# Optimization experiments

Hardware: AMD Instinct MI355X
Metric: run time of the kernel (lower is better)

The kernel has to match this reference:

```python
import jax, jax.numpy as jnp
import numpy as np

B, S, HID = 2, 4096, 640
NH, NKV, HD = 4, 1, 256
SCALING = 256.0 ** -0.5
SOFTCAP = 50.0
WINDOW = 512
EPS = 1e-6
ROPE_THETA = 10000.0  # local (sliding) rope base in Gemma3


def _rope_tables(seq_len, dim, theta):
    inv_freq = 1.0 / (theta ** (np.arange(0, dim, 2, dtype=np.float32) / dim))  # [dim/2]
    t = np.arange(seq_len, dtype=np.float32)
    freqs = np.outer(t, inv_freq)                      # [S, dim/2]
    emb = np.concatenate([freqs, freqs], axis=-1)      # [S, dim]
    return np.cos(emb)[None], np.sin(emb)[None]        # [1, S, dim]


def _sliding_causal_mask(b, s, window):
    i = np.arange(s)[:, None]
    j = np.arange(s)[None, :]
    allowed = (j <= i) & (j > i - window)              # causal + sliding window
    mask = np.where(allowed, 0.0, -1e9).astype(np.float32)
    return np.broadcast_to(mask[None, None], (b, 1, s, s)).copy()


def setup_inputs() -> dict:
    key = jax.random.key(0)
    ks = jax.random.split(key, 8)
    cos_np, sin_np = _rope_tables(S, HD, ROPE_THETA)
    return {
        "hidden_states": jax.random.normal(ks[0], (B, S, HID), jnp.float32),
        "cos": jnp.asarray(cos_np),
        "sin": jnp.asarray(sin_np),
        "attention_mask": jnp.asarray(_sliding_causal_mask(B, S, WINDOW)),
        "Wq": jax.random.normal(ks[1], (HID, NH * HD), jnp.float32) * 0.02,
        "Wk": jax.random.normal(ks[2], (HID, NKV * HD), jnp.float32) * 0.02,
        "Wv": jax.random.normal(ks[3], (HID, NKV * HD), jnp.float32) * 0.02,
        "Wo": jax.random.normal(ks[4], (NH * HD, HID), jnp.float32) * 0.02,
        "q_norm_w": jax.random.normal(ks[5], (HD,), jnp.float32) * 0.02,
        "k_norm_w": jax.random.normal(ks[6], (HD,), jnp.float32) * 0.02,
    }


def _rms_norm(x, w):
    var = jnp.mean(jnp.square(x), axis=-1, keepdims=True)
    return x * jax.lax.rsqrt(var + EPS) * (1.0 + w)


def _rotate_half(x):
    x1, x2 = jnp.split(x, 2, axis=-1)
    return jnp.concatenate([-x2, x1], axis=-1)


def _apply_rope(x, cos, sin):
    # x: [B, H, S, D]; cos/sin: [1, S, D] -> unsqueeze head dim
    c = cos[:, None, :, :]
    s = sin[:, None, :, :]
    return x * c + _rotate_half(x) * s


def reference(hidden_states, cos, sin, attention_mask, Wq, Wk, Wv, Wo, q_norm_w, k_norm_w):
    b, s, _ = hidden_states.shape
    # projections (no bias)
    q = (hidden_states @ Wq).reshape(b, s, NH, HD).transpose(0, 2, 1, 3)   # [B,NH,S,D]
    k = (hidden_states @ Wk).reshape(b, s, NKV, HD).transpose(0, 2, 1, 3)  # [B,1,S,D]
    v = (hidden_states @ Wv).reshape(b, s, NKV, HD).transpose(0, 2, 1, 3)  # [B,1,S,D]
    # per-head RMSNorm on q/k
    q = _rms_norm(q, q_norm_w)
    k = _rms_norm(k, k_norm_w)
    # RoPE
    q = _apply_rope(q, cos, sin)
    k = _apply_rope(k, cos, sin)
    # GQA: single kv head broadcast to all query heads
    k2 = k[:, 0]  # [B,S,D]
    v2 = v[:, 0]  # [B,S,D]
    scores = jnp.einsum('bhqd,bkd->bhqk', q, k2) * SCALING
    scores = SOFTCAP * jnp.tanh(scores / SOFTCAP)          # logit softcapping
    scores = scores + attention_mask                        # causal + sliding window
    attn = jax.nn.softmax(scores, axis=-1)
    out = jnp.einsum('bhqk,bkd->bhqd', attn, v2)            # [B,NH,S,D]
    out = out.transpose(0, 2, 1, 3).reshape(b, s, NH * HD)  # [B,S,NH*D]
    return out @ Wo                                         # [B,S,HID]
```

## Files before the change

### kernel.cpp

```cpp
#include <hip/hip_runtime.h>

typedef unsigned short u16;
typedef unsigned int u32;

typedef __attribute__((ext_vector_type(8)))  short bf16x8;
typedef __attribute__((ext_vector_type(4)))  float f32x4;

__device__ __forceinline__ float b2f(u16 u) {
    union { unsigned int i; float f; } v; v.i = ((unsigned int)u) << 16; return v.f;
}
__device__ __forceinline__ u16 f2b(float f) {
    union { float ff; unsigned int i; } v; v.ff = f;
    unsigned int x = v.i;
    return (u16)((x + 0x7fffu + ((x >> 16) & 1u)) >> 16);
}
__device__ __forceinline__ bool detect_bf16(const void* cosT) {
    return ((*(const u32*)cosT) & 0xffffu) == 0x3f80u;
}
__device__ __forceinline__ float4 ld4(const void* p, size_t off, bool isbf) {
    if (isbf) {
        ushort4 v = *(const ushort4*)((const u16*)p + off);
        return make_float4(b2f(v.x), b2f(v.y), b2f(v.z), b2f(v.w));
    }
    return *(const float4*)((const float*)p + off);
}
__device__ __forceinline__ float lds1(const void* p, size_t off, bool isbf) {
    return isbf ? b2f(((const u16*)p)[off]) : ((const float*)p)[off];
}
__device__ __forceinline__ void gll16(const void* g, void* l) {
    __builtin_amdgcn_global_load_lds(
        (const __attribute__((address_space(1))) u32*)g,
        (__attribute__((address_space(3))) u32*)l, 16, 0, 0);
}
__device__ __forceinline__ float capmask(float sdot, int i, int j) {
    float v = sdot * (0.0625f / 50.0f);
    v = fminf(fmaxf(v, -10.0f), 10.0f);
    float e = __expf(2.0f * v);
    float c = 50.0f * (e - 1.0f) / (e + 1.0f);
    bool allowed = (j <= i) && (j > i - 512);
    return allowed ? c : -1e30f;
}

__global__ __launch_bounds__(256) void conv_hidden(
    const void* __restrict__ src, const void* __restrict__ cosT, u16* __restrict__ dst)
{
    const bool isbf = detect_bf16(cosT);
    size_t base = ((size_t)blockIdx.x * 256 + threadIdx.x) * 8;
    if (isbf) {
        *(uint4*)(dst + base) = *(const uint4*)((const u16*)src + base);
    } else {
        float4 a = ld4(src, base, false);
        float4 b = ld4(src, base + 4, false);
        uint4 o;
        o.x = (u32)f2b(a.x) | ((u32)f2b(a.y) << 16);
        o.y = (u32)f2b(a.z) | ((u32)f2b(a.w) << 16);
        o.z = (u32)f2b(b.x) | ((u32)f2b(b.y) << 16);
        o.w = (u32)f2b(b.z) | ((u32)f2b(b.w) << 16);
        *(uint4*)(dst + base) = o;
    }
}

__global__ __launch_bounds__(256) void transpose_w(
    const void* __restrict__ Wq, const void* __restrict__ Wk,
    const void* __restrict__ Wv, const void* __restrict__ Wo,
    const void* __restrict__ cosT,
    u16* __restrict__ WT, u16* __restrict__ WoT)
{
    const bool isbf = detect_bf16(cosT);
    __shared__ float T[32][33];
    const int tx = threadIdx.x & 31, ty = threadIdx.x >> 5;
    int id = blockIdx.x;
    if (id < 960) {
        const int n0 = (id % 48) * 32, k0 = (id / 48) * 32;
        const void* src; int ldw, nof;
        if (n0 < 1024)      { src = Wq; ldw = 1024; nof = n0; }
        else if (n0 < 1280) { src = Wk; ldw = 256;  nof = n0 - 1024; }
        else                { src = Wv; ldw = 256;  nof = n0 - 1280; }
#pragma unroll
        for (int j = 0; j < 4; j++)
            T[ty + 8 * j][tx] = lds1(src, (size_t)(k0 + ty + 8 * j) * ldw + nof + tx, isbf);
        __syncthreads();
#pragma unroll
        for (int j = 0; j < 4; j++)
            WT[(size_t)(n0 + ty + 8 * j) * 640 + k0 + tx] = f2b(T[tx][ty + 8 * j]);
    } else {
        id -= 960;
        const int k0 = (id & 31) * 32, n0 = (id >> 5) * 32;
#pragma unroll
        for (int j = 0; j < 4; j++)
            T[ty + 8 * j][tx] = lds1(Wo, (size_t)(k0 + ty + 8 * j) * 640 + n0 + tx, isbf);
        __syncthreads();
#pragma unroll
        for (int j = 0; j < 4; j++)
            WoT[(size_t)(n0 + ty + 8 * j) * 1024 + k0 + tx] = f2b(T[tx][ty + 8 * j]);
    }
}

__global__ __launch_bounds__(256) void qkv_gemm(
    const u16* __restrict__ Hb, const u16* __restrict__ WT,
    u16* __restrict__ Qb, u16* __restrict__ Kb, u16* __restrict__ Vtg)
{
    const int n0 = blockIdx.x * 128, m0 = blockIdx.y * 128;
    const int t = threadIdx.x, w = t >> 6, lane = t & 63;
    const int l15 = lane & 15, quad = lane >> 4;
    const int wm = (w & 1) * 64, wn = (w >> 1) * 64;

    __shared__ __align__(16) u16 Ah[128][32];
    __shared__ __align__(16) u16 Bh[128][32];

    f32x4 acc[4][4];
#pragma unroll
    for (int i = 0; i < 4; i++)
#pragma unroll
        for (int j = 0; j < 4; j++) acc[i][j] = (f32x4)0.0f;

    for (int kb = 0; kb < 640; kb += 32) {
        __syncthreads();
#pragma unroll
        for (int i = 0; i < 2; i++) {
            int ci = t + 256 * i, m = ci >> 2, c = ci & 3;
            gll16(Hb + (size_t)(m0 + m) * 640 + kb + c * 8, (char*)&Ah[0][0] + ci * 16);
            gll16(WT + (size_t)(n0 + m) * 640 + kb + c * 8, (char*)&Bh[0][0] + ci * 16);
        }
        __syncthreads();
        bf16x8 af[4], bfr[4];
#pragma unroll
        for (int mi = 0; mi < 4; mi++)
            af[mi] = *(const bf16x8*)&Ah[wm + mi * 16 + l15][quad * 8];
#pragma unroll
        for (int ni = 0; ni < 4; ni++)
            bfr[ni] = *(const bf16x8*)&Bh[wn + ni * 16 + l15][quad * 8];
#pragma unroll
        for (int mi = 0; mi < 4; mi++)
#pragma unroll
            for (int ni = 0; ni < 4; ni++)
                acc[mi][ni] = __builtin_amdgcn_mfma_f32_16x16x32_bf16(
                    af[mi], bfr[ni], acc[mi][ni], 0, 0, 0);
    }

    const int bb = m0 >> 12, sblk = m0 & 4095;
#pragma unroll
    for (int mi = 0; mi < 4; mi++)
#pragma unroll
        for (int ni = 0; ni < 4; ni++) {
            int rowb = m0 + wm + mi * 16 + quad * 4;
            int col  = n0 + wn + ni * 16 + l15;
            if (n0 < 1024) {
#pragma unroll
                for (int r = 0; r < 4; r++)
                    Qb[(size_t)(rowb + r) * 1024 + col] = f2b(acc[mi][ni][r]);
            } else if (n0 < 1280) {
#pragma unroll
                for (int r = 0; r < 4; r++)
                    Kb[(size_t)(rowb + r) * 256 + (col - 1024)] = f2b(acc[mi][ni][r]);
            } else {
                int vd = col - 1280;
                int sb = sblk + wm + mi * 16 + quad * 4;
                ushort4 vv = make_ushort4(f2b(acc[mi][ni][0]), f2b(acc[mi][ni][1]),
                                          f2b(acc[mi][ni][2]), f2b(acc[mi][ni][3]));
                *(ushort4*)(Vtg + (size_t)bb * 1048576 + (size_t)vd * 4096 + sb) = vv;
            }
        }
}

__global__ __launch_bounds__(320) void norm_rope(
    u16* __restrict__ Qb, u16* __restrict__ Kb,
    const void* __restrict__ cosT, const void* __restrict__ sinT,
    const void* __restrict__ qw, const void* __restrict__ kw)
{
    const bool isbf = detect_bf16(cosT);
    const int row = blockIdx.x, s = row & 4095;
    const int g = threadIdx.x >> 6, lane = threadIdx.x & 63, d0 = lane * 4;

    u16* p; const void* w;
    if (g < 4) { p = Qb + (size_t)row * 1024 + g * 256 + d0; w = qw; }
    else       { p = Kb + (size_t)row * 256 + d0;            w = kw; }

    ushort4 xv = *(const ushort4*)p;
    float x0 = b2f(xv.x), x1 = b2f(xv.y), x2 = b2f(xv.z), x3 = b2f(xv.w);
    float ssum = x0 * x0 + x1 * x1 + x2 * x2 + x3 * x3;
#pragma unroll
    for (int off = 32; off > 0; off >>= 1) ssum += __shfl_xor(ssum, off, 64);
    float rs = rsqrtf(ssum * (1.0f / 256.0f) + 1e-6f);

    float4 wv = ld4(w, d0, isbf);
    float n0 = x0 * rs * (1.0f + wv.x);
    float n1 = x1 * rs * (1.0f + wv.y);
    float n2 = x2 * rs * (1.0f + wv.z);
    float n3 = x3 * rs * (1.0f + wv.w);

    float o0 = __shfl_xor(n0, 32, 64);
    float o1 = __shfl_xor(n1, 32, 64);
    float o2 = __shfl_xor(n2, 32, 64);
    float o3 = __shfl_xor(n3, 32, 64);
    float sgn = (lane < 32) ? -1.0f : 1.0f;

    float4 cv = ld4(cosT, (size_t)s * 256 + d0, isbf);
    float4 sv = ld4(sinT, (size_t)s * 256 + d0, isbf);
    *(ushort4*)p = make_ushort4(
        f2b(n0 * cv.x + sgn * o0 * sv.x), f2b(n1 * cv.y + sgn * o1 * sv.y),
        f2b(n2 * cv.z + sgn * o2 * sv.z), f2b(n3 * cv.w + sgn * o3 * sv.w));
}

__global__ __launch_bounds__(256, 2) void attn_mfma(
    const u16* __restrict__ Qb, const u16* __restrict__ Kb,
    const u16* __restrict__ Vtg, u16* __restrict__ AO)
{
    const int q0 = blockIdx.x * 16;
    const int b  = blockIdx.y;
    const int t = threadIdx.x, h = t >> 6, lane = t & 63;
    const int l15 = lane & 15, quad = lane >> 4;

    __shared__ __align__(16) u16 Ks[32][264];
    __shared__ __align__(16) u16 Vt[256][40];
    __shared__ __align__(16) u16 Pr[4][16][40];
    __shared__ float l_s[4][16];

    bf16x8 qf[8];
    {
        const u16* qp = Qb + ((size_t)(b * 4096 + q0 + l15)) * 1024 + h * 256 + quad * 8;
#pragma unroll
        for (int s = 0; s < 8; s++) qf[s] = *(const bf16x8*)(qp + s * 32);
    }

    f32x4 o[16];
#pragma unroll
    for (int i = 0; i < 16; i++) o[i] = (f32x4)0.0f;
    float lp[4] = {0.f, 0.f, 0.f, 0.f};

    int lo = q0 - 511;
    const int jb0 = lo > 0 ? (lo >> 5) << 5 : 0;
    const int jb1 = (q0 + 15) & ~31;
    for (int jb = jb0; jb <= jb1; jb += 32) {
        __syncthreads();
#pragma unroll
        for (int i = 0; i < 4; i++) {
            int ci = t + 256 * i;
            int key = ci >> 5, c = ci & 31;
            *(uint4*)&Ks[key][c * 8] =
                *(const uint4*)(Kb + ((size_t)(b * 4096 + jb + key)) * 256 + c * 8);
            int d = ci >> 2, c2 = ci & 3;
            *(uint4*)&Vt[d][c2 * 8] =
                *(const uint4*)(Vtg + (size_t)b * 1048576 + (size_t)d * 4096 + jb + c2 * 8);
        }
        __syncthreads();

        f32x4 s0 = (f32x4)0.0f, s1 = (f32x4)0.0f;
#pragma unroll
        for (int ds = 0; ds < 8; ds++) {
            bf16x8 kf0 = *(const bf16x8*)&Ks[l15][ds * 32 + quad * 8];
            bf16x8 kf1 = *(const bf16x8*)&Ks[16 + l15][ds * 32 + quad * 8];
            s0 = __builtin_amdgcn_mfma_f32_16x16x32_bf16(qf[ds], kf0, s0, 0, 0, 0);
            s1 = __builtin_amdgcn_mfma_f32_16x16x32_bf16(qf[ds], kf1, s1, 0, 0, 0);
        }
        const int j0 = jb + l15;
#pragma unroll
        for (int r = 0; r < 4; r++) {
            int qi = q0 + quad * 4 + r;
            float p0 = __expf(capmask(s0[r], qi, j0));
            float p1 = __expf(capmask(s1[r], qi, j0 + 16));
            u16 pb0 = f2b(p0), pb1 = f2b(p1);
            Pr[h][quad * 4 + r][l15]      = pb0;
            Pr[h][quad * 4 + r][16 + l15] = pb1;
            lp[r] += b2f(pb0) + b2f(pb1);
        }
        __threadfence_block();
#pragma unroll
        for (int mt = 0; mt < 16; mt++) {
            bf16x8 vf = *(const bf16x8*)&Vt[mt * 16 + l15][quad * 8];
            bf16x8 pf = *(const bf16x8*)&Pr[h][l15][quad * 8];
            o[mt] = __builtin_amdgcn_mfma_f32_16x16x32_bf16(vf, pf, o[mt], 0, 0, 0);
        }
    }

#pragma unroll
    for (int r = 0; r < 4; r++) {
        float v = lp[r];
        v += __shfl_xor(v, 1, 64); v += __shfl_xor(v, 2, 64);
        v += __shfl_xor(v, 4, 64); v += __shfl_xor(v, 8, 64);
        lp[r] = v;
    }
    if (l15 == 0) {
#pragma unroll
        for (int r = 0; r < 4; r++) l_s[h][quad * 4 + r] = lp[r];
    }
    __threadfence_block();
    __syncthreads();
    const float inv = 1.0f / l_s[h][l15];

    u16* aop = AO + ((size_t)(b * 4096 + q0 + l15)) * 1024 + h * 256 + quad * 4;
#pragma unroll
    for (int mt = 0; mt < 16; mt++) {
        *(ushort4*)(aop + mt * 16) = make_ushort4(
            f2b(o[mt][0] * inv), f2b(o[mt][1] * inv),
            f2b(o[mt][2] * inv), f2b(o[mt][3] * inv));
    }
}

__global__ __launch_bounds__(256) void out_gemm(
    const u16* __restrict__ AO, const u16* __restrict__ WoT,
    const void* __restrict__ cosT, void* __restrict__ outp)
{
    const bool isbf = detect_bf16(cosT);
    const int n0 = blockIdx.x * 128, m0 = blockIdx.y * 128;
    const int t = threadIdx.x, w = t >> 6, lane = t & 63;
    const int l15 = lane & 15, quad = lane >> 4;
    const int wm = (w & 1) * 64, wn = (w >> 1) * 64;

    __shared__ __align__(16) u16 Ah[128][32];
    __shared__ __align__(16) u16 Bh[128][32];

    f32x4 acc[4][4];
#pragma unroll
    for (int i = 0; i < 4; i++)
#pragma unroll
        for (int j = 0; j < 4; j++) acc[i][j] = (f32x4)0.0f;

    for (int kb = 0; kb < 1024; kb += 32) {
        __syncthreads();
#pragma unroll
        for (int i = 0; i < 2; i++) {
            int ci = t + 256 * i, m = ci >> 2, c = ci & 3;
            gll16(AO + (size_t)(m0 + m) * 1024 + kb + c * 8, (char*)&Ah[0][0] + ci * 16);
            gll16(WoT + (size_t)(n0 + m) * 1024 + kb + c * 8, (char*)&Bh[0][0] + ci * 16);
        }
        __syncthreads();
        bf16x8 af[4], bfr[4];
#pragma unroll
        for (int mi = 0; mi < 4; mi++)
            af[mi] = *(const bf16x8*)&Ah[wm + mi * 16 + l15][quad * 8];
#pragma unroll
        for (int ni = 0; ni < 4; ni++)
            bfr[ni] = *(const bf16x8*)&Bh[wn + ni * 16 + l15][quad * 8];
#pragma unroll
        for (int mi = 0; mi < 4; mi++)
#pragma unroll
            for (int ni = 0; ni < 4; ni++)
                acc[mi][ni] = __builtin_amdgcn_mfma_f32_16x16x32_bf16(
                    af[mi], bfr[ni], acc[mi][ni], 0, 0, 0);
    }

#pragma unroll
    for (int mi = 0; mi < 4; mi++)
#pragma unroll
        for (int ni = 0; ni < 4; ni++) {
            int rowb = m0 + wm + mi * 16 + quad * 4;
            int col  = n0 + wn + ni * 16 + l15;
            if (isbf) {
#pragma unroll
                for (int r = 0; r < 4; r++)
                    ((u16*)outp)[(size_t)(rowb + r) * 640 + col] = f2b(acc[mi][ni][r]);
            } else {
#pragma unroll
                for (int r = 0; r < 4; r++)
                    ((float*)outp)[(size_t)(rowb + r) * 640 + col] = acc[mi][ni][r];
            }
        }
}

extern "C" void kernel_launch(void* const* d_in, const int* in_sizes, int n_in,
                              void* d_out, int out_size, void* d_ws, size_t ws_size,
                              hipStream_t stream) {
    const void* hidden = d_in[0];
    const void* cosT   = d_in[1];
    const void* sinT   = d_in[2];
    const void* Wq     = d_in[4];
    const void* Wk     = d_in[5];
    const void* Wv     = d_in[6];
    const void* Wo     = d_in[7];
    const void* qw     = d_in[8];
    const void* kw     = d_in[9];

    char* ws = (char*)d_ws;
    u16* Hb  = (u16*)ws;
    u16* WT  = (u16*)(ws + 10485760);
    u16* AO  = (u16*)ws;
    u16* WoT = (u16*)(ws + 16777216);
    u16* Qb  = (u16*)(ws + 18087936);
    u16* Kb  = (u16*)(ws + 34865152);
    u16* Vtg = (u16*)(ws + 39059456);

    conv_hidden<<<dim3(2560), 256, 0, stream>>>(hidden, cosT, Hb);
    transpose_w<<<dim3(1600), 256, 0, stream>>>(Wq, Wk, Wv, Wo, cosT, WT, WoT);
    qkv_gemm<<<dim3(12, 64), 256, 0, stream>>>(Hb, WT, Qb, Kb, Vtg);
    norm_rope<<<dim3(8192), 320, 0, stream>>>(Qb, Kb, cosT, sinT, qw, kw);
    attn_mfma<<<dim3(256, 2), 256, 0, stream>>>(Qb, Kb, Vtg, AO);
    out_gemm<<<dim3(5, 64), 256, 0, stream>>>(AO, WoT, cosT, d_out);
}
```

Measured before the change: 340.7 us.

## Fuse prep kernels, fold Q norm+RoPE into attention, prefetch K/V, retile out GEMM

Merges the hidden-state conversion and weight transposes into one prep launch. Moves the Q RMSNorm and RoPE into the attention kernel's Q load, leaving a smaller K-only norm/rope kernel. Adds register prefetch of the next K/V tile in the attention loop and raises its occupancy hint to 3 blocks. Halves the out-GEMM N tile to launch more blocks. These changes cut launches and global round trips for Q, at the cost of extra register pressure in the attention kernel.

```diff
diff --git a/kernel.cpp b/kernel.cpp
--- a/kernel.cpp
+++ b/kernel.cpp
@@ -41,35 +41,34 @@
     return allowed ? c : -1e30f;
 }
 
-__global__ __launch_bounds__(256) void conv_hidden(
-    const void* __restrict__ src, const void* __restrict__ cosT, u16* __restrict__ dst)
-{
-    const bool isbf = detect_bf16(cosT);
-    size_t base = ((size_t)blockIdx.x * 256 + threadIdx.x) * 8;
-    if (isbf) {
-        *(uint4*)(dst + base) = *(const uint4*)((const u16*)src + base);
-    } else {
-        float4 a = ld4(src, base, false);
-        float4 b = ld4(src, base + 4, false);
-        uint4 o;
-        o.x = (u32)f2b(a.x) | ((u32)f2b(a.y) << 16);
-        o.y = (u32)f2b(a.z) | ((u32)f2b(a.w) << 16);
-        o.z = (u32)f2b(b.x) | ((u32)f2b(b.y) << 16);
-        o.w = (u32)f2b(b.z) | ((u32)f2b(b.w) << 16);
-        *(uint4*)(dst + base) = o;
-    }
-}
-
-__global__ __launch_bounds__(256) void transpose_w(
+__global__ __launch_bounds__(256) void prep(
+    const void* __restrict__ hidden,
     const void* __restrict__ Wq, const void* __restrict__ Wk,
     const void* __restrict__ Wv, const void* __restrict__ Wo,
     const void* __restrict__ cosT,
-    u16* __restrict__ WT, u16* __restrict__ WoT)
+    u16* __restrict__ Hb, u16* __restrict__ WT, u16* __restrict__ WoT)
 {
     const bool isbf = detect_bf16(cosT);
     __shared__ float T[32][33];
+    int id = blockIdx.x;
+    if (id < 2560) {
+        size_t base = ((size_t)id * 256 + threadIdx.x) * 8;
+        if (isbf) {
+            *(uint4*)(Hb + base) = *(const uint4*)((const u16*)hidden + base);
+        } else {
+            float4 a = ld4(hidden, base, false);
+            float4 b = ld4(hidden, base + 4, false);
+            uint4 o;
+            o.x = (u32)f2b(a.x) | ((u32)f2b(a.y) << 16);
+            o.y = (u32)f2b(a.z) | ((u32)f2b(a.w) << 16);
+            o.z = (u32)f2b(b.x) | ((u32)f2b(b.y) << 16);
+            o.w = (u32)f2b(b.z) | ((u32)f2b(b.w) << 16);
+            *(uint4*)(Hb + base) = o;
+        }
+        return;
+    }
+    id -= 2560;
     const int tx = threadIdx.x & 31, ty = threadIdx.x >> 5;
-    int id = blockIdx.x;
     if (id < 960) {
         const int n0 = (id % 48) * 32, k0 = (id / 48) * 32;
         const void* src; int ldw, nof;
@@ -163,19 +162,16 @@
         }
 }
 
-__global__ __launch_bounds__(320) void norm_rope(
-    u16* __restrict__ Qb, u16* __restrict__ Kb,
+__global__ __launch_bounds__(64) void k_norm_rope(
+    u16* __restrict__ Kb,
     const void* __restrict__ cosT, const void* __restrict__ sinT,
-    const void* __restrict__ qw, const void* __restrict__ kw)
+    const void* __restrict__ kw)
 {
     const bool isbf = detect_bf16(cosT);
     const int row = blockIdx.x, s = row & 4095;
-    const int g = threadIdx.x >> 6, lane = threadIdx.x & 63, d0 = lane * 4;
-
-    u16* p; const void* w;
-    if (g < 4) { p = Qb + (size_t)row * 1024 + g * 256 + d0; w = qw; }
-    else       { p = Kb + (size_t)row * 256 + d0;            w = kw; }
-
+    const int lane = threadIdx.x, d0 = lane * 4;
+
+    u16* p = Kb + (size_t)row * 256 + d0;
     ushort4 xv = *(const ushort4*)p;
     float x0 = b2f(xv.x), x1 = b2f(xv.y), x2 = b2f(xv.z), x3 = b2f(xv.w);
     float ssum = x0 * x0 + x1 * x1 + x2 * x2 + x3 * x3;
@@ -183,7 +179,7 @@
     for (int off = 32; off > 0; off >>= 1) ssum += __shfl_xor(ssum, off, 64);
     float rs = rsqrtf(ssum * (1.0f / 256.0f) + 1e-6f);
 
-    float4 wv = ld4(w, d0, isbf);
+    float4 wv = ld4(kw, d0, isbf);
     float n0 = x0 * rs * (1.0f + wv.x);
     float n1 = x1 * rs * (1.0f + wv.y);
     float n2 = x2 * rs * (1.0f + wv.z);
@@ -202,10 +198,13 @@
         f2b(n2 * cv.z + sgn * o2 * sv.z), f2b(n3 * cv.w + sgn * o3 * sv.w));
 }
 
-__global__ __launch_bounds__(256, 2) void attn_mfma(
+__global__ __launch_bounds__(256, 3) void attn_mfma(
     const u16* __restrict__ Qb, const u16* __restrict__ Kb,
-    const u16* __restrict__ Vtg, u16* __restrict__ AO)
+    const u16* __restrict__ Vtg,
+    const void* __restrict__ cosT, const void* __restrict__ sinT,
+    const void* __restrict__ qw, u16* __restrict__ AO)
 {
+    const bool isbf = detect_bf16(cosT);
     const int q0 = blockIdx.x * 16;
     const int b  = blockIdx.y;
     const int t = threadIdx.x, h = t >> 6, lane = t & 63;
@@ -221,6 +220,40 @@
         const u16* qp = Qb + ((size_t)(b * 4096 + q0 + l15)) * 1024 + h * 256 + quad * 8;
 #pragma unroll
         for (int s = 0; s < 8; s++) qf[s] = *(const bf16x8*)(qp + s * 32);
+        float ss = 0.f;
+#pragma unroll
+        for (int s = 0; s < 8; s++)
+#pragma unroll
+            for (int j = 0; j < 8; j++) { float v = b2f((u16)qf[s][j]); ss += v * v; }
+        ss += __shfl_xor(ss, 16, 64);
+        ss += __shfl_xor(ss, 32, 64);
+        const float rs = rsqrtf(ss * (1.0f / 256.0f) + 1e-6f);
+        const size_t crow = (size_t)(q0 + l15) * 256;
+#pragma unroll
+        for (int sp = 0; sp < 4; sp++) {
+            const int da = quad * 8 + sp * 32, db = da + 128;
+            float4 w0 = ld4(qw, da, isbf),        w1 = ld4(qw, da + 4, isbf);
+            float4 u0 = ld4(qw, db, isbf),        u1 = ld4(qw, db + 4, isbf);
+            float4 ca0 = ld4(cosT, crow + da, isbf), ca1 = ld4(cosT, crow + da + 4, isbf);
+            float4 cb0 = ld4(cosT, crow + db, isbf), cb1 = ld4(cosT, crow + db + 4, isbf);
+            float4 sa0 = ld4(sinT, crow + da, isbf), sa1 = ld4(sinT, crow + da + 4, isbf);
+            float4 sb0 = ld4(sinT, crow + db, isbf), sb1 = ld4(sinT, crow + db + 4, isbf);
+            float wa[8] = {w0.x,w0.y,w0.z,w0.w,w1.x,w1.y,w1.z,w1.w};
+            float wb[8] = {u0.x,u0.y,u0.z,u0.w,u1.x,u1.y,u1.z,u1.w};
+            float ca[8] = {ca0.x,ca0.y,ca0.z,ca0.w,ca1.x,ca1.y,ca1.z,ca1.w};
+            float cb[8] = {cb0.x,cb0.y,cb0.z,cb0.w,cb1.x,cb1.y,cb1.z,cb1.w};
+            float sa[8] = {sa0.x,sa0.y,sa0.z,sa0.w,sa1.x,sa1.y,sa1.z,sa1.w};
+            float sb[8] = {sb0.x,sb0.y,sb0.z,sb0.w,sb1.x,sb1.y,sb1.z,sb1.w};
+            bf16x8 outa, outb;
+#pragma unroll
+            for (int j = 0; j < 8; j++) {
+                float na = b2f((u16)qf[sp][j])     * rs * (1.0f + wa[j]);
+                float nb = b2f((u16)qf[sp + 4][j]) * rs * (1.0f + wb[j]);
+                outa[j] = (short)f2b(na * ca[j] - nb * sa[j]);
+                outb[j] = (short)f2b(nb * cb[j] + na * sb[j]);
+            }
+            qf[sp] = outa; qf[sp + 4] = outb;
+        }
     }
 
     f32x4 o[16];
@@ -228,22 +261,39 @@
     for (int i = 0; i < 16; i++) o[i] = (f32x4)0.0f;
     float lp[4] = {0.f, 0.f, 0.f, 0.f};
 
-    int lo = q0 - 511;
+    const int lo = q0 - 511;
     const int jb0 = lo > 0 ? (lo >> 5) << 5 : 0;
     const int jb1 = (q0 + 15) & ~31;
+
+    const u16* kbase = Kb + (size_t)b * 4096 * 256;
+    const u16* vbase = Vtg + (size_t)b * 1048576;
+
+    uint4 kreg[4], vreg[4];
+#pragma unroll
+    for (int i = 0; i < 4; i++) {
+        int ci = t + 256 * i;
+        kreg[i] = *(const uint4*)(kbase + (size_t)(jb0 + (ci >> 5)) * 256 + (ci & 31) * 8);
+        vreg[i] = *(const uint4*)(vbase + (size_t)(ci >> 2) * 4096 + jb0 + (ci & 3) * 8);
+    }
+
     for (int jb = jb0; jb <= jb1; jb += 32) {
         __syncthreads();
 #pragma unroll
         for (int i = 0; i < 4; i++) {
             int ci = t + 256 * i;
-            int key = ci >> 5, c = ci & 31;
-            *(uint4*)&Ks[key][c * 8] =
-                *(const uint4*)(Kb + ((size_t)(b * 4096 + jb + key)) * 256 + c * 8);
-            int d = ci >> 2, c2 = ci & 3;
-            *(uint4*)&Vt[d][c2 * 8] =
-                *(const uint4*)(Vtg + (size_t)b * 1048576 + (size_t)d * 4096 + jb + c2 * 8);
-        }
-        __syncthreads();
+            *(uint4*)&Ks[ci >> 5][(ci & 31) * 8] = kreg[i];
+            *(uint4*)&Vt[ci >> 2][(ci & 3) * 8]  = vreg[i];
+        }
+        __syncthreads();
+        if (jb + 32 <= jb1) {
+            const int jn = jb + 32;
+#pragma unroll
+            for (int i = 0; i < 4; i++) {
+                int ci = t + 256 * i;
+                kreg[i] = *(const uint4*)(kbase + (size_t)(jn + (ci >> 5)) * 256 + (ci & 31) * 8);
+                vreg[i] = *(const uint4*)(vbase + (size_t)(ci >> 2) * 4096 + jn + (ci & 3) * 8);
+            }
+        }
 
         f32x4 s0 = (f32x4)0.0f, s1 = (f32x4)0.0f;
 #pragma unroll
@@ -302,19 +352,19 @@
     const void* __restrict__ cosT, void* __restrict__ outp)
 {
     const bool isbf = detect_bf16(cosT);
-    const int n0 = blockIdx.x * 128, m0 = blockIdx.y * 128;
+    const int n0 = blockIdx.x * 64, m0 = blockIdx.y * 128;
     const int t = threadIdx.x, w = t >> 6, lane = t & 63;
     const int l15 = lane & 15, quad = lane >> 4;
-    const int wm = (w & 1) * 64, wn = (w >> 1) * 64;
+    const int wm = (w & 1) * 64, wn = (w >> 1) * 32;
 
     __shared__ __align__(16) u16 Ah[128][32];
-    __shared__ __align__(16) u16 Bh[128][32];
-
-    f32x4 acc[4][4];
+    __shared__ __align__(16) u16 Bh[64][32];
+
+    f32x4 acc[4][2];
 #pragma unroll
     for (int i = 0; i < 4; i++)
 #pragma unroll
-        for (int j = 0; j < 4; j++) acc[i][j] = (f32x4)0.0f;
+        for (int j = 0; j < 2; j++) acc[i][j] = (f32x4)0.0f;
 
     for (int kb = 0; kb < 1024; kb += 32) {
         __syncthreads();
@@ -322,20 +372,23 @@
         for (int i = 0; i < 2; i++) {
             int ci = t + 256 * i, m = ci >> 2, c = ci & 3;
             gll16(AO + (size_t)(m0 + m) * 1024 + kb + c * 8, (char*)&Ah[0][0] + ci * 16);
-            gll16(WoT + (size_t)(n0 + m) * 1024 + kb + c * 8, (char*)&Bh[0][0] + ci * 16);
-        }
-        __syncthreads();
-        bf16x8 af[4], bfr[4];
+        }
+        {
+            int m = t >> 2, c = t & 3;
+            gll16(WoT + (size_t)(n0 + m) * 1024 + kb + c * 8, (char*)&Bh[0][0] + t * 16);
+        }
+        __syncthreads();
+        bf16x8 af[4], bfr[2];
 #pragma unroll
         for (int mi = 0; mi < 4; mi++)
             af[mi] = *(const bf16x8*)&Ah[wm + mi * 16 + l15][quad * 8];
 #pragma unroll
-        for (int ni = 0; ni < 4; ni++)
+        for (int ni = 0; ni < 2; ni++)
             bfr[ni] = *(const bf16x8*)&Bh[wn + ni * 16 + l15][quad * 8];
 #pragma unroll
         for (int mi = 0; mi < 4; mi++)
 #pragma unroll
-            for (int ni = 0; ni < 4; ni++)
+            for (int ni = 0; ni < 2; ni++)
                 acc[mi][ni] = __builtin_amdgcn_mfma_f32_16x16x32_bf16(
                     af[mi], bfr[ni], acc[mi][ni], 0, 0, 0);
     }
@@ -343,7 +396,7 @@
 #pragma unroll
     for (int mi = 0; mi < 4; mi++)
 #pragma unroll
-        for (int ni = 0; ni < 4; ni++) {
+        for (int ni = 0; ni < 2; ni++) {
             int rowb = m0 + wm + mi * 16 + quad * 4;
             int col  = n0 + wn + ni * 16 + l15;
             if (isbf) {
@@ -380,10 +433,9 @@
     u16* Kb  = (u16*)(ws + 34865152);
     u16* Vtg = (u16*)(ws + 39059456);
 
-    conv_hidden<<<dim3(2560), 256, 0, stream>>>(hidden, cosT, Hb);
-    transpose_w<<<dim3(1600), 256, 0, stream>>>(Wq, Wk, Wv, Wo, cosT, WT, WoT);
+    prep<<<dim3(4160), 256, 0, stream>>>(hidden, Wq, Wk, Wv, Wo, cosT, Hb, WT, WoT);
     qkv_gemm<<<dim3(12, 64), 256, 0, stream>>>(Hb, WT, Qb, Kb, Vtg);
-    norm_rope<<<dim3(8192), 320, 0, stream>>>(Qb, Kb, cosT, sinT, qw, kw);
-    attn_mfma<<<dim3(256, 2), 256, 0, stream>>>(Qb, Kb, Vtg, AO);
-    out_gemm<<<dim3(5, 64), 256, 0, stream>>>(AO, WoT, cosT, d_out);
-}
+    k_norm_rope<<<dim3(8192), 64, 0, stream>>>(Kb, cosT, sinT, kw);
+    attn_mfma<<<dim3(256, 2), 256, 0, stream>>>(Qb, Kb, Vtg, cosT, sinT, qw, AO);
+    out_gemm<<<dim3(10, 64), 256, 0, stream>>>(AO, WoT, cosT, d_out);
+}
```

Result: slower. 417.4 us (+22.5%).
